# Kernel tuning notes

Measured on AMD Instinct MI355X. Metric: run time of the kernel, lower is better.

Reference implementation:

```python
import jax, jax.numpy as jnp
import numpy as np

S, B, IN, H = 512, 128, 256, 512  # seq_len, batch, input_size, hidden_size


def setup_inputs() -> dict:
    key = jax.random.key(0)
    ks = jax.random.split(key, 17)
    def p(k, shape):
        return jax.random.normal(k, shape, dtype=jnp.float32) * 0.05
    inp = {
        "x": jax.random.normal(ks[0], (S, B, IN), dtype=jnp.float32),
        "h0": jnp.zeros((1, B, H), dtype=jnp.float32),
        "c0": jnp.zeros((1, B, H), dtype=jnp.float32),
    }
    # gates: f=forget, i=input, o=output, g=cell candidate
    for j, n in enumerate(["f", "i", "o", "g"]):
        inp[f"W{n}"] = p(ks[1 + 4 * j], (H, IN))
        inp[f"bW{n}"] = p(ks[2 + 4 * j], (H,))
        inp[f"U{n}"] = p(ks[3 + 4 * j], (H, H))
        inp[f"bU{n}"] = p(ks[4 + 4 * j], (H,))
    return inp


def reference(x, h0, c0, Wf, bWf, Uf, bUf, Wi, bWi, Ui, bUi,
              Wo, bWo, Uo, bUo, Wg, bWg, Ug, bUg):
    # Fuse the 4 input projections and 4 recurrent projections into single GEMMs.
    # Math is identical to applying each Linear separately.
    Wcat = jnp.concatenate([Wf, Wi, Wo, Wg], axis=0)      # [4H, IN]
    bcat = jnp.concatenate([bWf + bUf, bWi + bUi, bWo + bUo, bWg + bUg])  # [4H]
    Ucat = jnp.concatenate([Uf, Ui, Uo, Ug], axis=0)      # [4H, H]
    hd = h0.shape[-1]
    # Precompute input-dependent gate pre-activations for all timesteps.
    xg = jnp.einsum('sbi,gi->sbg', x, Wcat) + bcat        # [S, B, 4H]

    def step(carry, xg_t):
        h, c = carry
        g = xg_t + h @ Ucat.T                             # [B, 4H]
        f = jax.nn.sigmoid(g[..., :hd])
        i = jax.nn.sigmoid(g[..., hd:2 * hd])
        o = jax.nn.sigmoid(g[..., 2 * hd:3 * hd])
        cand = jnp.tanh(g[..., 3 * hd:])
        c = f * c + i * cand
        h = o * jnp.tanh(c)
        return (h, c), h

    (h, c), h_seq = jax.lax.scan(step, (h0[-1], c0[-1]), xg)
    return h_seq, h, c
```

## Files before the change

kernel.cpp:

```cpp
#include <hip/hip_runtime.h>
#include <hip/hip_cooperative_groups.h>

namespace cg = cooperative_groups;


#define SQ   512
#define BB   128
#define IN_  256
#define HH   512
#define RG   8
#define CGN  32
#define RINGHALF (BB * HH)
#define RING_OFF 1024

typedef float    f32x4 __attribute__((ext_vector_type(4)));
typedef short    s16x8 __attribute__((ext_vector_type(8)));
typedef unsigned u32x4 __attribute__((ext_vector_type(4)));

struct P {
  const float *x, *h0, *c0;
  const float *W[4], *bW[4], *U[4], *bU[4];
  float* out;
  unsigned* ring;
  int mode;
};

__device__ __forceinline__ unsigned f2b(float f) {
  unsigned u = __float_as_uint(f);
  return (u + 0x7FFFu + ((u >> 16) & 1u)) >> 16;
}
__device__ __forceinline__ float sigm(float x) { return 1.f / (1.f + __expf(-x)); }
__device__ __forceinline__ float tanh_(float x) {
  float e = __expf(-2.f * fabsf(x));
  float t = (1.f - e) / (1.f + e);
  return copysignf(t, x);
}
__device__ __forceinline__ u32x4 pack8(f32x4 a, f32x4 b) {
  u32x4 d;
  d.x = f2b(a.x) | (f2b(a.y) << 16);
  d.y = f2b(a.z) | (f2b(a.w) << 16);
  d.z = f2b(b.x) | (f2b(b.y) << 16);
  d.w = f2b(b.z) | (f2b(b.w) << 16);
  return d;
}
__device__ __forceinline__ unsigned mergelo(unsigned d0, unsigned d1) {
  return __builtin_amdgcn_perm(d1, d0, 0x05040100u);
}

#define LOAD8_LLC(c0_,c1_,c2_,c3_,c4_,c5_,c6_,c7_,ptr_)                      \
  asm volatile(                                                              \
    "global_load_dwordx4 %0, %8, off sc0 sc1\n\t"                            \
    "global_load_dwordx4 %1, %8, off offset:256 sc0 sc1\n\t"                 \
    "global_load_dwordx4 %2, %8, off offset:512 sc0 sc1\n\t"                 \
    "global_load_dwordx4 %3, %8, off offset:768 sc0 sc1\n\t"                 \
    "global_load_dwordx4 %4, %8, off offset:1024 sc0 sc1\n\t"                \
    "global_load_dwordx4 %5, %8, off offset:1280 sc0 sc1\n\t"                \
    "global_load_dwordx4 %6, %8, off offset:1536 sc0 sc1\n\t"                \
    "global_load_dwordx4 %7, %8, off offset:1792 sc0 sc1\n\t"                \
    "s_waitcnt vmcnt(0)"                                                     \
    : "=&v"(c0_), "=&v"(c1_), "=&v"(c2_), "=&v"(c3_),                        \
      "=&v"(c4_), "=&v"(c5_), "=&v"(c6_), "=&v"(c7_)                         \
    : "v"(ptr_) : "memory")

__global__ void __launch_bounds__(256, 1) lstm_all(P p) {
  __shared__ unsigned short Hs[16][512];
  __shared__ unsigned short Xs[2][16][256];
  __shared__ float gbuf[4][16][17];

  const int tid = threadIdx.x;
  const int bid = blockIdx.x;
  const int r   = bid & 7;
  const int cgi = bid >> 3;
  const int rb  = r * 16;
  const int hcb = cgi * 16;

  const int w   = tid >> 6;
  const int l   = tid & 63;
  const int l16 = l & 15;
  const int lk  = l >> 4;
  const int row16 = tid >> 4;
  const int n16   = tid & 15;

  unsigned* ring = p.ring;

  const int col = hcb + l16;
  s16x8 bfrag[24];
#pragma unroll
  for (int kk = 0; kk < 24; ++kk) {
    int k = kk * 32 + lk * 8;
    const float* src = (kk < 8) ? (p.W[w] + (size_t)col * IN_ + k)
                                : (p.U[w] + (size_t)col * HH + (k - IN_));
    f32x4 a = *(const f32x4*)src;
    f32x4 b = *(const f32x4*)(src + 4);
    s16x8 v;
    v[0]=(short)f2b(a.x); v[1]=(short)f2b(a.y); v[2]=(short)f2b(a.z); v[3]=(short)f2b(a.w);
    v[4]=(short)f2b(b.x); v[5]=(short)f2b(b.y); v[6]=(short)f2b(b.z); v[7]=(short)f2b(b.w);
    bfrag[kk] = v;
  }
  const float bias = p.bW[w][col] + p.bU[w][col];
  float cval = p.c0[(size_t)(rb + row16) * HH + hcb + n16];

  const int wswz = (row16 & 7) << 4;
  const int rswz = (l16 & 7) << 4;
  char* HsB = (char*)&Hs[0][0];
  char* XsB = (char*)&Xs[0][0][0];

  f32x4 xg0, xg1, xg2, xg3;
  {
    const float* xs = p.x + (size_t)(rb + row16) * IN_ + n16 * 16;
    xg0 = *(const f32x4*)(xs);
    xg1 = *(const f32x4*)(xs + 4);
    xg2 = *(const f32x4*)(xs + 8);
    xg3 = *(const f32x4*)(xs + 12);
  }

  for (int t = 0; t < SQ; ++t) {
    {
      char* xrow = XsB + (t & 1) * 8192 + row16 * 512;
      *(u32x4*)(xrow + ((n16 * 32)      ^ wswz)) = pack8(xg0, xg1);
      *(u32x4*)(xrow + ((n16 * 32 + 16) ^ wswz)) = pack8(xg2, xg3);
      if (t + 1 < SQ) {
        const float* xs = p.x + ((size_t)(t + 1) * BB + rb + row16) * IN_ + n16 * 16;
        xg0 = *(const f32x4*)(xs);
        xg1 = *(const f32x4*)(xs + 4);
        xg2 = *(const f32x4*)(xs + 8);
        xg3 = *(const f32x4*)(xs + 12);
      }
    }

    char* hrow = HsB + row16 * 1024;
    if (t == 0) {
      const float* src = p.h0 + (size_t)(rb + row16) * HH + n16 * 4;
#pragma unroll
      for (int cc = 0; cc < 8; ++cc) {
        f32x4 v = *(const f32x4*)(src + cc * 64);
        unsigned lo = f2b(v.x) | (f2b(v.y) << 16);
        unsigned hi = f2b(v.z) | (f2b(v.w) << 16);
        int boff = ((cc * 128 + n16 * 8) ^ wswz);
        *(uint2*)(hrow + boff) = make_uint2(lo, hi);
      }
    } else if (p.mode == 0) {
      const unsigned* hb = ring + (((t - 1) & 1) ? RINGHALF : 0)
                         + (size_t)(rb + row16) * HH + n16 * 4;
      u32x4 c0,c1,c2,c3,c4,c5,c6,c7;
      const unsigned tg = (unsigned)t;
#define TAGOK(v) (((v).x >> 16) == tg && ((v).y >> 16) == tg && \
                  ((v).z >> 16) == tg && ((v).w >> 16) == tg)
      int spin = 0;
      for (;;) {
        LOAD8_LLC(c0,c1,c2,c3,c4,c5,c6,c7,hb);
        if (TAGOK(c0) && TAGOK(c1) && TAGOK(c2) && TAGOK(c3) &&
            TAGOK(c4) && TAGOK(c5) && TAGOK(c6) && TAGOK(c7)) break;
        if (++spin > (1 << 16)) break;
        if (spin > 8) __builtin_amdgcn_s_sleep(1);
      }
#undef TAGOK
      u32x4 cv[8] = {c0,c1,c2,c3,c4,c5,c6,c7};
#pragma unroll
      for (int cc = 0; cc < 8; ++cc) {
        uint2 u = make_uint2(mergelo(cv[cc].x, cv[cc].y),
                             mergelo(cv[cc].z, cv[cc].w));
        int boff = ((cc * 128 + n16 * 8) ^ wswz);
        *(uint2*)(hrow + boff) = u;
      }
    } else {
      cg::this_grid().sync();
      const float* hp = p.out + ((size_t)(t - 1) * BB + rb + row16) * HH + n16 * 4;
      u32x4 a0,a1,a2,a3,a4,a5,a6,a7;
      LOAD8_LLC(a0,a1,a2,a3,a4,a5,a6,a7,hp);
      u32x4 av[8] = {a0,a1,a2,a3,a4,a5,a6,a7};
#pragma unroll
      for (int cc = 0; cc < 8; ++cc) {
        unsigned lo = f2b(__uint_as_float(av[cc].x)) | (f2b(__uint_as_float(av[cc].y)) << 16);
        unsigned hi = f2b(__uint_as_float(av[cc].z)) | (f2b(__uint_as_float(av[cc].w)) << 16);
        int boff = ((cc * 128 + n16 * 8) ^ wswz);
        *(uint2*)(hrow + boff) = make_uint2(lo, hi);
      }
    }
    __syncthreads();

    f32x4 acc0 = { bias, bias, bias, bias };
    f32x4 acc1 = { 0.f, 0.f, 0.f, 0.f };
    f32x4 acc2 = { 0.f, 0.f, 0.f, 0.f };
    f32x4 acc3 = { 0.f, 0.f, 0.f, 0.f };
    const char* xr = XsB + (t & 1) * 8192 + l16 * 512;
    const char* hr = HsB + l16 * 1024;
#pragma unroll
    for (int kp = 0; kp < 8; kp += 4) {
      s16x8 a0 = *(const s16x8*)(xr + (((kp + 0) * 64 + lk * 16) ^ rswz));
      s16x8 a1 = *(const s16x8*)(xr + (((kp + 1) * 64 + lk * 16) ^ rswz));
      s16x8 a2 = *(const s16x8*)(xr + (((kp + 2) * 64 + lk * 16) ^ rswz));
      s16x8 a3 = *(const s16x8*)(xr + (((kp + 3) * 64 + lk * 16) ^ rswz));
      acc0 = __builtin_amdgcn_mfma_f32_16x16x32_bf16(a0, bfrag[kp],     acc0, 0, 0, 0);
      acc1 = __builtin_amdgcn_mfma_f32_16x16x32_bf16(a1, bfrag[kp + 1], acc1, 0, 0, 0);
      acc2 = __builtin_amdgcn_mfma_f32_16x16x32_bf16(a2, bfrag[kp + 2], acc2, 0, 0, 0);
      acc3 = __builtin_amdgcn_mfma_f32_16x16x32_bf16(a3, bfrag[kp + 3], acc3, 0, 0, 0);
    }
#pragma unroll
    for (int kp = 0; kp < 16; kp += 4) {
      s16x8 a0 = *(const s16x8*)(hr + (((kp + 0) * 64 + lk * 16) ^ rswz));
      s16x8 a1 = *(const s16x8*)(hr + (((kp + 1) * 64 + lk * 16) ^ rswz));
      s16x8 a2 = *(const s16x8*)(hr + (((kp + 2) * 64 + lk * 16) ^ rswz));
      s16x8 a3 = *(const s16x8*)(hr + (((kp + 3) * 64 + lk * 16) ^ rswz));
      acc0 = __builtin_amdgcn_mfma_f32_16x16x32_bf16(a0, bfrag[8 + kp],  acc0, 0, 0, 0);
      acc1 = __builtin_amdgcn_mfma_f32_16x16x32_bf16(a1, bfrag[9 + kp],  acc1, 0, 0, 0);
      acc2 = __builtin_amdgcn_mfma_f32_16x16x32_bf16(a2, bfrag[10 + kp], acc2, 0, 0, 0);
      acc3 = __builtin_amdgcn_mfma_f32_16x16x32_bf16(a3, bfrag[11 + kp], acc3, 0, 0, 0);
    }

#pragma unroll
    for (int rr = 0; rr < 4; ++rr) {
      float v = (acc0[rr] + acc1[rr]) + (acc2[rr] + acc3[rr]);
      v = (w < 3) ? sigm(v) : tanh_(v);
      gbuf[w][lk * 4 + rr][l16] = v;
    }
    __syncthreads();

    float f = gbuf[0][row16][n16];
    float i = gbuf[1][row16][n16];
    float o = gbuf[2][row16][n16];
    float g = gbuf[3][row16][n16];
    cval = f * cval + i * g;
    float h = o * tanh_(cval);

    size_t oidx = ((size_t)t * BB + rb + row16) * HH + hcb + n16;
    if (p.mode == 0) {
      unsigned tw = ((unsigned)(t + 1) << 16) | f2b(h);
      unsigned* dst = ring + ((t & 1) ? RINGHALF : 0)
                    + (size_t)(rb + row16) * HH + hcb + n16;
      asm volatile("global_store_dword %0, %1, off sc0 sc1"
                   :: "v"(dst), "v"(tw) : "memory");
      __builtin_nontemporal_store(h, p.out + oidx);
    } else {
      asm volatile("global_store_dword %0, %1, off sc0 sc1"
                   :: "v"(p.out + oidx), "v"(h) : "memory");
      asm volatile("s_waitcnt vmcnt(0)" ::: "memory");
    }
    if (t == SQ - 1) {
      size_t base = (size_t)SQ * BB * HH;
      size_t idx2 = (size_t)(rb + row16) * HH + hcb + n16;
      p.out[base + idx2] = h;
      p.out[base + (size_t)BB * HH + idx2] = cval;
    }
  }
}

extern "C" void kernel_launch(void* const* d_in, const int* in_sizes, int n_in,
                              void* d_out, int out_size, void* d_ws, size_t ws_size,
                              hipStream_t stream) {
  P p;
  p.x  = (const float*)d_in[0];
  p.h0 = (const float*)d_in[1];
  p.c0 = (const float*)d_in[2];
  for (int g = 0; g < 4; ++g) {
    p.W[g]  = (const float*)d_in[3 + 4 * g];
    p.bW[g] = (const float*)d_in[4 + 4 * g];
    p.U[g]  = (const float*)d_in[5 + 4 * g];
    p.bU[g] = (const float*)d_in[6 + 4 * g];
  }
  p.out = (float*)d_out;

  const size_t need = (size_t)(RING_OFF + 2 * BB * HH) * sizeof(unsigned);
  const bool ws_ok = (d_ws != nullptr) && (ws_size >= need);
  p.mode = ws_ok ? 0 : 2;
  p.ring = ws_ok ? ((unsigned*)d_ws + RING_OFF) : nullptr;
  if (ws_ok) hipMemsetAsync(d_ws, 0, need, stream);

  void* args[] = { &p };
  hipError_t e = hipLaunchCooperativeKernel((const void*)lstm_all,
                                            dim3(RG * CGN), dim3(256),
                                            args, 0, stream);
  if (e != hipSuccess) {
    hipLaunchKernelGGL(lstm_all, dim3(RG * CGN), dim3(256), 0, stream, p);
  }
}
```

Baseline: 1.291 ms.

## Halve grid to 128 blocks, each processing two 16-row batch slots per step

Each workgroup now owns two 16-row batch tiles instead of one, so the grid drops from 256 to 128 blocks. The per-block weight fragments held in registers are reused across both slots, and the recurrence work for the two slots runs back to back within each timestep. This reduces the number of blocks taking part in the cross-block spin-wait handoff and the duplicated weight loading. In exchange, each block does twice the serial work per timestep, only half the CUs are used, and the second slot's sync waits are not overlapped with the first slot's compute.

Result: slower. 2.476 ms (+91.8%).

```diff
diff --git a/kernel.cpp b/kernel.cpp
--- a/kernel.cpp
+++ b/kernel.cpp
@@ -8,7 +8,6 @@
 #define BB   128
 #define IN_  256
 #define HH   512
-#define RG   8
 #define CGN  32
 #define RINGHALF (BB * HH)
 #define RING_OFF 1024
@@ -62,16 +61,153 @@
       "=&v"(c4_), "=&v"(c5_), "=&v"(c6_), "=&v"(c7_)                         \
     : "v"(ptr_) : "memory")
 
+template <int S>
+__device__ __forceinline__ void slot(const P& p, unsigned* ring, int t,
+    int rbS, float& cval,
+    f32x4& X0, f32x4& X1, f32x4& X2, f32x4& X3,
+    char* HsB, char* XsB, float* gb,
+    int row16, int n16, int l16, int lk, int w, int hcb,
+    int wswz, int rswz, const s16x8* bfrag, float bias) {
+  {
+    char* xrow = XsB + S * 16384 + (t & 1) * 8192 + row16 * 512;
+    *(u32x4*)(xrow + ((n16 * 32)      ^ wswz)) = pack8(X0, X1);
+    *(u32x4*)(xrow + ((n16 * 32 + 16) ^ wswz)) = pack8(X2, X3);
+    if (t + 1 < SQ) {
+      const float* xs = p.x + ((size_t)(t + 1) * BB + rbS + row16) * IN_ + n16 * 16;
+      X0 = *(const f32x4*)(xs);
+      X1 = *(const f32x4*)(xs + 4);
+      X2 = *(const f32x4*)(xs + 8);
+      X3 = *(const f32x4*)(xs + 12);
+    }
+  }
+
+  char* hrow = HsB + S * 16384 + row16 * 1024;
+  if (t == 0) {
+    const float* src = p.h0 + (size_t)(rbS + row16) * HH + n16 * 4;
+#pragma unroll
+    for (int cc = 0; cc < 8; ++cc) {
+      f32x4 v = *(const f32x4*)(src + cc * 64);
+      unsigned lo = f2b(v.x) | (f2b(v.y) << 16);
+      unsigned hi = f2b(v.z) | (f2b(v.w) << 16);
+      int boff = ((cc * 128 + n16 * 8) ^ wswz);
+      *(uint2*)(hrow + boff) = make_uint2(lo, hi);
+    }
+  } else if (p.mode == 0) {
+    const unsigned* hb = ring + (((t - 1) & 1) ? RINGHALF : 0)
+                       + (size_t)(rbS + row16) * HH + n16 * 4;
+    u32x4 c0, c1, c2, c3, c4, c5, c6, c7;
+    const unsigned tg = (unsigned)t;
+#define TAGOK(v) (((v).x >> 16) == tg && ((v).y >> 16) == tg && \
+                  ((v).z >> 16) == tg && ((v).w >> 16) == tg)
+    int spin = 0;
+    for (;;) {
+      LOAD8_LLC(c0, c1, c2, c3, c4, c5, c6, c7, hb);
+      if (TAGOK(c0) && TAGOK(c1) && TAGOK(c2) && TAGOK(c3) &&
+          TAGOK(c4) && TAGOK(c5) && TAGOK(c6) && TAGOK(c7)) break;
+      if (++spin > (1 << 16)) break;
+      if (spin > 8) __builtin_amdgcn_s_sleep(1);
+    }
+#undef TAGOK
+    u32x4 cv[8] = {c0, c1, c2, c3, c4, c5, c6, c7};
+#pragma unroll
+    for (int cc = 0; cc < 8; ++cc) {
+      uint2 u = make_uint2(mergelo(cv[cc].x, cv[cc].y),
+                           mergelo(cv[cc].z, cv[cc].w));
+      int boff = ((cc * 128 + n16 * 8) ^ wswz);
+      *(uint2*)(hrow + boff) = u;
+    }
+  } else {
+    cg::this_grid().sync();
+    const float* hp = p.out + ((size_t)(t - 1) * BB + rbS + row16) * HH + n16 * 4;
+    u32x4 a0, a1, a2, a3, a4, a5, a6, a7;
+    LOAD8_LLC(a0, a1, a2, a3, a4, a5, a6, a7, hp);
+    u32x4 av[8] = {a0, a1, a2, a3, a4, a5, a6, a7};
+#pragma unroll
+    for (int cc = 0; cc < 8; ++cc) {
+      unsigned lo = f2b(__uint_as_float(av[cc].x)) | (f2b(__uint_as_float(av[cc].y)) << 16);
+      unsigned hi = f2b(__uint_as_float(av[cc].z)) | (f2b(__uint_as_float(av[cc].w)) << 16);
+      int boff = ((cc * 128 + n16 * 8) ^ wswz);
+      *(uint2*)(hrow + boff) = make_uint2(lo, hi);
+    }
+  }
+  __syncthreads();
+
+  f32x4 acc0 = { bias, bias, bias, bias };
+  f32x4 acc1 = { 0.f, 0.f, 0.f, 0.f };
+  f32x4 acc2 = { 0.f, 0.f, 0.f, 0.f };
+  f32x4 acc3 = { 0.f, 0.f, 0.f, 0.f };
+  const char* xr = XsB + S * 16384 + (t & 1) * 8192 + l16 * 512;
+  const char* hr = HsB + S * 16384 + l16 * 1024;
+#pragma unroll
+  for (int kp = 0; kp < 8; kp += 4) {
+    s16x8 a0 = *(const s16x8*)(xr + (((kp + 0) * 64 + lk * 16) ^ rswz));
+    s16x8 a1 = *(const s16x8*)(xr + (((kp + 1) * 64 + lk * 16) ^ rswz));
+    s16x8 a2 = *(const s16x8*)(xr + (((kp + 2) * 64 + lk * 16) ^ rswz));
+    s16x8 a3 = *(const s16x8*)(xr + (((kp + 3) * 64 + lk * 16) ^ rswz));
+    acc0 = __builtin_amdgcn_mfma_f32_16x16x32_bf16(a0, bfrag[kp],     acc0, 0, 0, 0);
+    acc1 = __builtin_amdgcn_mfma_f32_16x16x32_bf16(a1, bfrag[kp + 1], acc1, 0, 0, 0);
+    acc2 = __builtin_amdgcn_mfma_f32_16x16x32_bf16(a2, bfrag[kp + 2], acc2, 0, 0, 0);
+    acc3 = __builtin_amdgcn_mfma_f32_16x16x32_bf16(a3, bfrag[kp + 3], acc3, 0, 0, 0);
+  }
+#pragma unroll
+  for (int kp = 0; kp < 16; kp += 4) {
+    s16x8 a0 = *(const s16x8*)(hr + (((kp + 0) * 64 + lk * 16) ^ rswz));
+    s16x8 a1 = *(const s16x8*)(hr + (((kp + 1) * 64 + lk * 16) ^ rswz));
+    s16x8 a2 = *(const s16x8*)(hr + (((kp + 2) * 64 + lk * 16) ^ rswz));
+    s16x8 a3 = *(const s16x8*)(hr + (((kp + 3) * 64 + lk * 16) ^ rswz));
+    acc0 = __builtin_amdgcn_mfma_f32_16x16x32_bf16(a0, bfrag[8 + kp],  acc0, 0, 0, 0);
+    acc1 = __builtin_amdgcn_mfma_f32_16x16x32_bf16(a1, bfrag[9 + kp],  acc1, 0, 0, 0);
+    acc2 = __builtin_amdgcn_mfma_f32_16x16x32_bf16(a2, bfrag[10 + kp], acc2, 0, 0, 0);
+    acc3 = __builtin_amdgcn_mfma_f32_16x16x32_bf16(a3, bfrag[11 + kp], acc3, 0, 0, 0);
+  }
+
+#pragma unroll
+  for (int rr = 0; rr < 4; ++rr) {
+    float v = (acc0[rr] + acc1[rr]) + (acc2[rr] + acc3[rr]);
+    v = (w < 3) ? sigm(v) : tanh_(v);
+    gb[w * 272 + (lk * 4 + rr) * 17 + l16] = v;
+  }
+  __syncthreads();
+
+  float f = gb[0 * 272 + row16 * 17 + n16];
+  float i = gb[1 * 272 + row16 * 17 + n16];
+  float o = gb[2 * 272 + row16 * 17 + n16];
+  float g = gb[3 * 272 + row16 * 17 + n16];
+  cval = f * cval + i * g;
+  float h = o * tanh_(cval);
+
+  size_t oidx = ((size_t)t * BB + rbS + row16) * HH + hcb + n16;
+  if (p.mode == 0) {
+    unsigned tw = ((unsigned)(t + 1) << 16) | f2b(h);
+    unsigned* dst = ring + ((t & 1) ? RINGHALF : 0)
+                  + (size_t)(rbS + row16) * HH + hcb + n16;
+    asm volatile("global_store_dword %0, %1, off sc0 sc1"
+                 :: "v"(dst), "v"(tw) : "memory");
+    __builtin_nontemporal_store(h, p.out + oidx);
+  } else {
+    asm volatile("global_store_dword %0, %1, off sc0 sc1"
+                 :: "v"(p.out + oidx), "v"(h) : "memory");
+    asm volatile("s_waitcnt vmcnt(0)" ::: "memory");
+  }
+  if (t == SQ - 1) {
+    size_t base = (size_t)SQ * BB * HH;
+    size_t idx2 = (size_t)(rbS + row16) * HH + hcb + n16;
+    p.out[base + idx2] = h;
+    p.out[base + (size_t)BB * HH + idx2] = cval;
+  }
+}
+
 __global__ void __launch_bounds__(256, 1) lstm_all(P p) {
-  __shared__ unsigned short Hs[16][512];
-  __shared__ unsigned short Xs[2][16][256];
+  __shared__ unsigned short Hs[2][16][512];
+  __shared__ unsigned short Xs[2][2][16][256];
   __shared__ float gbuf[4][16][17];
 
   const int tid = threadIdx.x;
   const int bid = blockIdx.x;
-  const int r   = bid & 7;
-  const int cgi = bid >> 3;
-  const int rb  = r * 16;
+  const int pr  = bid & 3;
+  const int cgi = bid >> 2;
+  const int rbA = pr * 32;
+  const int rbB = pr * 32 + 16;
   const int hcb = cgi * 16;
 
   const int w   = tid >> 6;
@@ -98,150 +234,34 @@
     bfrag[kk] = v;
   }
   const float bias = p.bW[w][col] + p.bU[w][col];
-  float cval = p.c0[(size_t)(rb + row16) * HH + hcb + n16];
+  float cvalA = p.c0[(size_t)(rbA + row16) * HH + hcb + n16];
+  float cvalB = p.c0[(size_t)(rbB + row16) * HH + hcb + n16];
 
   const int wswz = (row16 & 7) << 4;
   const int rswz = (l16 & 7) << 4;
-  char* HsB = (char*)&Hs[0][0];
-  char* XsB = (char*)&Xs[0][0][0];
-
-  f32x4 xg0, xg1, xg2, xg3;
+  char* HsB = (char*)&Hs[0][0][0];
+  char* XsB = (char*)&Xs[0][0][0][0];
+  float* gb = &gbuf[0][0][0];
+
+  f32x4 xA0, xA1, xA2, xA3, xB0, xB1, xB2, xB3;
   {
-    const float* xs = p.x + (size_t)(rb + row16) * IN_ + n16 * 16;
-    xg0 = *(const f32x4*)(xs);
-    xg1 = *(const f32x4*)(xs + 4);
-    xg2 = *(const f32x4*)(xs + 8);
-    xg3 = *(const f32x4*)(xs + 12);
+    const float* xa = p.x + (size_t)(rbA + row16) * IN_ + n16 * 16;
+    xA0 = *(const f32x4*)(xa);
+    xA1 = *(const f32x4*)(xa + 4);
+    xA2 = *(const f32x4*)(xa + 8);
+    xA3 = *(const f32x4*)(xa + 12);
+    const float* xb = p.x + (size_t)(rbB + row16) * IN_ + n16 * 16;
+    xB0 = *(const f32x4*)(xb);
+    xB1 = *(const f32x4*)(xb + 4);
+    xB2 = *(const f32x4*)(xb + 8);
+    xB3 = *(const f32x4*)(xb + 12);
   }
 
   for (int t = 0; t < SQ; ++t) {
-    {
-      char* xrow = XsB + (t & 1) * 8192 + row16 * 512;
-      *(u32x4*)(xrow + ((n16 * 32)      ^ wswz)) = pack8(xg0, xg1);
-      *(u32x4*)(xrow + ((n16 * 32 + 16) ^ wswz)) = pack8(xg2, xg3);
-      if (t + 1 < SQ) {
-        const float* xs = p.x + ((size_t)(t + 1) * BB + rb + row16) * IN_ + n16 * 16;
-        xg0 = *(const f32x4*)(xs);
-        xg1 = *(const f32x4*)(xs + 4);
-        xg2 = *(const f32x4*)(xs + 8);
-        xg3 = *(const f32x4*)(xs + 12);
-      }
-    }
-
-    char* hrow = HsB + row16 * 1024;
-    if (t == 0) {
-      const float* src = p.h0 + (size_t)(rb + row16) * HH + n16 * 4;
-#pragma unroll
-      for (int cc = 0; cc < 8; ++cc) {
-        f32x4 v = *(const f32x4*)(src + cc * 64);
-        unsigned lo = f2b(v.x) | (f2b(v.y) << 16);
-        unsigned hi = f2b(v.z) | (f2b(v.w) << 16);
-        int boff = ((cc * 128 + n16 * 8) ^ wswz);
-        *(uint2*)(hrow + boff) = make_uint2(lo, hi);
-      }
-    } else if (p.mode == 0) {
-      const unsigned* hb = ring + (((t - 1) & 1) ? RINGHALF : 0)
-                         + (size_t)(rb + row16) * HH + n16 * 4;
-      u32x4 c0,c1,c2,c3,c4,c5,c6,c7;
-      const unsigned tg = (unsigned)t;
-#define TAGOK(v) (((v).x >> 16) == tg && ((v).y >> 16) == tg && \
-                  ((v).z >> 16) == tg && ((v).w >> 16) == tg)
-      int spin = 0;
-      for (;;) {
-        LOAD8_LLC(c0,c1,c2,c3,c4,c5,c6,c7,hb);
-        if (TAGOK(c0) && TAGOK(c1) && TAGOK(c2) && TAGOK(c3) &&
-            TAGOK(c4) && TAGOK(c5) && TAGOK(c6) && TAGOK(c7)) break;
-        if (++spin > (1 << 16)) break;
-        if (spin > 8) __builtin_amdgcn_s_sleep(1);
-      }
-#undef TAGOK
-      u32x4 cv[8] = {c0,c1,c2,c3,c4,c5,c6,c7};
-#pragma unroll
-      for (int cc = 0; cc < 8; ++cc) {
-        uint2 u = make_uint2(mergelo(cv[cc].x, cv[cc].y),
-                             mergelo(cv[cc].z, cv[cc].w));
-        int boff = ((cc * 128 + n16 * 8) ^ wswz);
-        *(uint2*)(hrow + boff) = u;
-      }
-    } else {
-      cg::this_grid().sync();
-      const float* hp = p.out + ((size_t)(t - 1) * BB + rb + row16) * HH + n16 * 4;
-      u32x4 a0,a1,a2,a3,a4,a5,a6,a7;
-      LOAD8_LLC(a0,a1,a2,a3,a4,a5,a6,a7,hp);
-      u32x4 av[8] = {a0,a1,a2,a3,a4,a5,a6,a7};
-#pragma unroll
-      for (int cc = 0; cc < 8; ++cc) {
-        unsigned lo = f2b(__uint_as_float(av[cc].x)) | (f2b(__uint_as_float(av[cc].y)) << 16);
-        unsigned hi = f2b(__uint_as_float(av[cc].z)) | (f2b(__uint_as_float(av[cc].w)) << 16);
-        int boff = ((cc * 128 + n16 * 8) ^ wswz);
-        *(uint2*)(hrow + boff) = make_uint2(lo, hi);
-      }
-    }
-    __syncthreads();
-
-    f32x4 acc0 = { bias, bias, bias, bias };
-    f32x4 acc1 = { 0.f, 0.f, 0.f, 0.f };
-    f32x4 acc2 = { 0.f, 0.f, 0.f, 0.f };
-    f32x4 acc3 = { 0.f, 0.f, 0.f, 0.f };
-    const char* xr = XsB + (t & 1) * 8192 + l16 * 512;
-    const char* hr = HsB + l16 * 1024;
-#pragma unroll
-    for (int kp = 0; kp < 8; kp += 4) {
-      s16x8 a0 = *(const s16x8*)(xr + (((kp + 0) * 64 + lk * 16) ^ rswz));
-      s16x8 a1 = *(const s16x8*)(xr + (((kp + 1) * 64 + lk * 16) ^ rswz));
-      s16x8 a2 = *(const s16x8*)(xr + (((kp + 2) * 64 + lk * 16) ^ rswz));
-      s16x8 a3 = *(const s16x8*)(xr + (((kp + 3) * 64 + lk * 16) ^ rswz));
-      acc0 = __builtin_amdgcn_mfma_f32_16x16x32_bf16(a0, bfrag[kp],     acc0, 0, 0, 0);
-      acc1 = __builtin_amdgcn_mfma_f32_16x16x32_bf16(a1, bfrag[kp + 1], acc1, 0, 0, 0);
-      acc2 = __builtin_amdgcn_mfma_f32_16x16x32_bf16(a2, bfrag[kp + 2], acc2, 0, 0, 0);
-      acc3 = __builtin_amdgcn_mfma_f32_16x16x32_bf16(a3, bfrag[kp + 3], acc3, 0, 0, 0);
-    }
-#pragma unroll
-    for (int kp = 0; kp < 16; kp += 4) {
-      s16x8 a0 = *(const s16x8*)(hr + (((kp + 0) * 64 + lk * 16) ^ rswz));
-      s16x8 a1 = *(const s16x8*)(hr + (((kp + 1) * 64 + lk * 16) ^ rswz));
-      s16x8 a2 = *(const s16x8*)(hr + (((kp + 2) * 64 + lk * 16) ^ rswz));
-      s16x8 a3 = *(const s16x8*)(hr + (((kp + 3) * 64 + lk * 16) ^ rswz));
-      acc0 = __builtin_amdgcn_mfma_f32_16x16x32_bf16(a0, bfrag[8 + kp],  acc0, 0, 0, 0);
-      acc1 = __builtin_amdgcn_mfma_f32_16x16x32_bf16(a1, bfrag[9 + kp],  acc1, 0, 0, 0);
-      acc2 = __builtin_amdgcn_mfma_f32_16x16x32_bf16(a2, bfrag[10 + kp], acc2, 0, 0, 0);
-      acc3 = __builtin_amdgcn_mfma_f32_16x16x32_bf16(a3, bfrag[11 + kp], acc3, 0, 0, 0);
-    }
-
-#pragma unroll
-    for (int rr = 0; rr < 4; ++rr) {
-      float v = (acc0[rr] + acc1[rr]) + (acc2[rr] + acc3[rr]);
-      v = (w < 3) ? sigm(v) : tanh_(v);
-      gbuf[w][lk * 4 + rr][l16] = v;
-    }
-    __syncthreads();
-
-    float f = gbuf[0][row16][n16];
-    float i = gbuf[1][row16][n16];
-    float o = gbuf[2][row16][n16];
-    float g = gbuf[3][row16][n16];
-    cval = f * cval + i * g;
-    float h = o * tanh_(cval);
-
-    size_t oidx = ((size_t)t * BB + rb + row16) * HH + hcb + n16;
-    if (p.mode == 0) {
-      unsigned tw = ((unsigned)(t + 1) << 16) | f2b(h);
-      unsigned* dst = ring + ((t & 1) ? RINGHALF : 0)
-                    + (size_t)(rb + row16) * HH + hcb + n16;
-      asm volatile("global_store_dword %0, %1, off sc0 sc1"
-                   :: "v"(dst), "v"(tw) : "memory");
-      __builtin_nontemporal_store(h, p.out + oidx);
-    } else {
-      asm volatile("global_store_dword %0, %1, off sc0 sc1"
-                   :: "v"(p.out + oidx), "v"(h) : "memory");
-      asm volatile("s_waitcnt vmcnt(0)" ::: "memory");
-    }
-    if (t == SQ - 1) {
-      size_t base = (size_t)SQ * BB * HH;
-      size_t idx2 = (size_t)(rb + row16) * HH + hcb + n16;
-      p.out[base + idx2] = h;
-      p.out[base + (size_t)BB * HH + idx2] = cval;
-    }
+    slot<0>(p, ring, t, rbA, cvalA, xA0, xA1, xA2, xA3,
+            HsB, XsB, gb, row16, n16, l16, lk, w, hcb, wswz, rswz, bfrag, bias);
+    slot<1>(p, ring, t, rbB, cvalB, xB0, xB1, xB2, xB3,
+            HsB, XsB, gb, row16, n16, l16, lk, w, hcb, wswz, rswz, bfrag, bias);
   }
 }
 
@@ -268,9 +288,9 @@
 
   void* args[] = { &p };
   hipError_t e = hipLaunchCooperativeKernel((const void*)lstm_all,
-                                            dim3(RG * CGN), dim3(256),
+                                            dim3(4 * CGN), dim3(256),
                                             args, 0, stream);
   if (e != hipSuccess) {
-    hipLaunchKernelGGL(lstm_all, dim3(RG * CGN), dim3(256), 0, stream, p);
-  }
-}
+    hipLaunchKernelGGL(lstm_all, dim3(4 * CGN), dim3(256), 0, stream, p);
+  }
+}
```
